# Kernel optimization log

Measured on AMD Instinct MI355X. Metric: run time of the kernel, lower is better.

The kernel has to match this reference:

```python
import jax, jax.numpy as jnp
import numpy as np

L, BS, D, NH = 1024, 4, 1024, 16
DH = D // NH
H = max(DH, L)  # big=True in DenseSynthesizer -> h = max(head_dim, n_tokens)


def setup_inputs() -> dict:
    key = jax.random.key(0)
    ks = jax.random.split(key, 10)
    s = 0.02
    x = jax.random.normal(ks[0], (L, BS, D), dtype=jnp.float32)
    # additive causal mask (n_tokens, n_tokens)
    causal = jnp.tril(jnp.ones((L, L), dtype=bool))
    attention_mask = jnp.where(causal, 0.0, -1e9).astype(jnp.float32)
    Wi = jax.random.normal(ks[1], (2 * D, D), dtype=jnp.float32) * s
    bi = jnp.zeros((2 * D,), dtype=jnp.float32)
    w1 = jax.random.normal(ks[2], (NH, DH, H), dtype=jnp.float32) * s
    b1 = jnp.zeros((NH, H), dtype=jnp.float32)
    w2 = jax.random.normal(ks[3], (NH, H, L), dtype=jnp.float32) * s
    b2 = jnp.zeros((NH, L), dtype=jnp.float32)
    Wo = jax.random.normal(ks[4], (D, D), dtype=jnp.float32) * s
    bo = jnp.zeros((D,), dtype=jnp.float32)
    return {"x": x, "attention_mask": attention_mask, "Wi": Wi, "bi": bi,
            "w1": w1, "b1": b1, "w2": w2, "b2": b2, "Wo": Wo, "bo": bo}


def reference(x, attention_mask, Wi, bi, w1, b1, w2, b2, Wo, bo):
    l, bs, d = x.shape
    nh, dh, h = w1.shape
    # input projection, chunk into synthesizer input q and values v
    proj = x @ Wi.T + bi                                    # (l, bs, 2d)
    q, v = jnp.split(proj, 2, axis=-1)
    q = q.reshape(l, bs, nh, dh).transpose(1, 0, 2, 3)      # (bs, l, nh, dh)
    v = v.reshape(l, bs * nh, dh).transpose(1, 0, 2)        # (bs*nh, l, dh), n = b*nh + k
    # DenseSynthesizer: per-head two-layer MLP producing attention logits
    hid = jax.nn.relu(jnp.einsum('blkd,kdh->blkh', q, w1) + b1)
    logits = jnp.einsum('blkh,khm->blkm', hid, w2) + b2     # (bs, l, nh, n_tokens)
    logits = logits[..., :l]
    # faithful to torch transpose(0,3).view(l,l,bs*nh).transpose(0,2):
    # flattened batch-head index is m = k*bs + b (head-major)
    logits = logits.transpose(2, 0, 1, 3).reshape(bs * nh, l, l)
    logits = logits + attention_mask[None, :, :]
    probs = jax.nn.softmax(logits, axis=-1)                 # dropout p=0 (eval)
    out = jnp.matmul(probs, v)                              # (bs*nh, l, dh)
    out = out.transpose(1, 0, 2).reshape(l, bs, d)
    return out @ Wo.T + bo
```

## Files before the change

### kernel.cpp

```cpp
#include <hip/hip_runtime.h>

typedef unsigned short u16;
typedef short bf16x8 __attribute__((ext_vector_type(8)));
typedef float f32x4 __attribute__((ext_vector_type(4)));

#define BSZ 4
#define DD 1024
#define LLL 1024

__device__ __forceinline__ float bf2f(u16 u) {
    union { unsigned int i; float f; } w;
    w.i = ((unsigned int)u) << 16;
    return w.f;
}
__device__ __forceinline__ u16 f2bf(float f) {
    union { float fl; unsigned int i; } w;
    w.fl = f;
    w.i += 0x7fffu + ((w.i >> 16) & 1u);
    return (u16)(w.i >> 16);
}

__device__ __forceinline__ void load_lds16(const u16* g, u16* l) {
    __builtin_amdgcn_global_load_lds(
        (const __attribute__((address_space(1))) unsigned int*)g,
        (__attribute__((address_space(3))) unsigned int*)l, 16, 0, 0);
}

__global__ void cvt_all(const float* __restrict__ x, const float* __restrict__ Wi,
                        const float* __restrict__ Wo, u16* __restrict__ xb,
                        u16* __restrict__ wib, u16* __restrict__ wob) {
    int b = blockIdx.x;
    const float* in; u16* out;
    if (b < 4096)      { in = x;  out = xb; }
    else if (b < 6144) { in = Wi; out = wib; b -= 4096; }
    else               { in = Wo; out = wob; b -= 6144; }
    const size_t i = ((size_t)b * 256 + threadIdx.x) * 4;
    const float4 v = *(const float4*)(in + i);
    ushort4 o;
    o.x = f2bf(v.x); o.y = f2bf(v.y); o.z = f2bf(v.z); o.w = f2bf(v.w);
    *(ushort4*)(out + i) = o;
}

__global__ void transpose_cvt(const float* __restrict__ in, u16* __restrict__ out,
                              int R, int C) {
    __shared__ float tile[32][33];
    const size_t base = (size_t)blockIdx.z * R * C;
    const int c0 = blockIdx.x << 5, r0 = blockIdx.y << 5;
    const int tx = threadIdx.x & 31, ty = threadIdx.x >> 5;
    #pragma unroll
    for (int i = 0; i < 32; i += 8)
        tile[ty + i][tx] = in[base + (size_t)(r0 + ty + i) * C + c0 + tx];
    __syncthreads();
    #pragma unroll
    for (int i = 0; i < 32; i += 8)
        out[base + (size_t)(c0 + ty + i) * R + r0 + tx] = f2bf(tile[tx][ty + i]);
}

__global__ void build_vt(const u16* __restrict__ proj, u16* __restrict__ vt) {
    __shared__ u16 tile[64][66];
    const int t = threadIdx.x;
    const int m0 = blockIdx.x << 6;
    const int jj = blockIdx.y;
    const int b = jj >> 4, k = jj & 15;
    const int tx = t & 63, ty = t >> 6;
    #pragma unroll
    for (int mi = ty; mi < 64; mi += 4)
        tile[mi][tx] = proj[(size_t)((m0 + mi) * BSZ + b) * 2048 + 1024 + k * 64 + tx];
    __syncthreads();
    #pragma unroll
    for (int di = ty; di < 64; di += 4)
        vt[((size_t)jj * 80 + di) * 1024 + m0 + tx] = tile[tx][di];
    #pragma unroll
    for (int di = 64 + ty; di < 80; di += 4)
        vt[((size_t)jj * 80 + di) * 1024 + m0 + tx] = (di == 64) ? 0x3F80 : 0;
}

template<int OUT_F32, int RELU>
__global__ __launch_bounds__(256, 2) void gemm_bf16_nt(
    const u16* __restrict__ A, int lda, long long sA,
    const u16* __restrict__ B, int ldb, long long sB,
    const float* __restrict__ bias, int sBias,
    void* __restrict__ C, int ldc, long long sC,
    int K)
{
    __shared__ u16 As[128 * 64];
    __shared__ u16 Bs[128 * 64];
    const int t = threadIdx.x;
    const int z = blockIdx.z;
    const u16* Ab = A + (size_t)z * sA + (size_t)blockIdx.x * 128 * lda;
    const u16* Bb = B + (size_t)z * sB + (size_t)blockIdx.y * 128 * ldb;
    const int wave = t >> 6, lane = t & 63;
    const int wrow = (wave >> 1) << 6;
    const int wcol = (wave & 1) << 6;
    const int lr = lane & 15, lq = lane >> 4;
    const int srow = t >> 3;
    const int gchunk = (t & 7) ^ (srow & 7);
    const u16* ApG = Ab + (size_t)srow * lda + gchunk * 8;
    const u16* BpG = Bb + (size_t)srow * ldb + gchunk * 8;
    u16* AsD = &As[t * 8];
    u16* BsD = &Bs[t * 8];
    const int o0 = ((lq    ) ^ (lr & 7)) * 8;
    const int o1 = ((lq + 4) ^ (lr & 7)) * 8;

    f32x4 acc[4][4];
    #pragma unroll
    for (int i = 0; i < 4; i++)
        #pragma unroll
        for (int j = 0; j < 4; j++)
            acc[i][j] = (f32x4){0.f, 0.f, 0.f, 0.f};

    for (int k0 = 0; k0 < K; k0 += 64) {
        __syncthreads();
        #pragma unroll
        for (int j = 0; j < 4; j++) {
            load_lds16(ApG + (size_t)j * 32 * lda + k0, AsD + j * 2048);
            load_lds16(BpG + (size_t)j * 32 * ldb + k0, BsD + j * 2048);
        }
        __syncthreads();
        #pragma unroll
        for (int s = 0; s < 2; s++) {
            const int oo = s ? o1 : o0;
            bf16x8 af[4], bfv[4];
            #pragma unroll
            for (int i = 0; i < 4; i++)
                af[i] = *(const bf16x8*)&As[(wrow + i * 16 + lr) * 64 + oo];
            #pragma unroll
            for (int j = 0; j < 4; j++)
                bfv[j] = *(const bf16x8*)&Bs[(wcol + j * 16 + lr) * 64 + oo];
            #pragma unroll
            for (int i = 0; i < 4; i++)
                #pragma unroll
                for (int j = 0; j < 4; j++)
                    acc[i][j] = __builtin_amdgcn_mfma_f32_16x16x32_bf16(
                        af[i], bfv[j], acc[i][j], 0, 0, 0);
        }
    }

    const float* biasb = bias + (size_t)z * sBias;
    const size_t row0 = (size_t)blockIdx.x * 128 + wrow + lq * 4;
    const int col0 = blockIdx.y * 128 + wcol + lr;
    #pragma unroll
    for (int j = 0; j < 4; j++) {
        const int col = col0 + j * 16;
        const float bb = biasb[col];
        #pragma unroll
        for (int i = 0; i < 4; i++) {
            #pragma unroll
            for (int r = 0; r < 4; r++) {
                const size_t row = row0 + i * 16 + r;
                float v = acc[i][j][r] + bb;
                if (RELU) v = fmaxf(v, 0.f);
                const size_t idx = row * (size_t)ldc + col;
                if (OUT_F32) ((float*)C)[(size_t)z * sC + idx] = v;
                else         ((u16*)C)[(size_t)z * sC + idx] = f2bf(v);
            }
        }
    }
}

__global__ __launch_bounds__(256, 2) void fused_attn(
    const u16* __restrict__ hid,
    const u16* __restrict__ w2t,
    const float* __restrict__ b2,
    const u16* __restrict__ vt,
    u16* __restrict__ attn)
{
    __shared__ u16 As[64 * 64];
    __shared__ u16 Bs[128 * 64];
    __shared__ u16 Ps[64 * 136];
    const int t = threadIdx.x;
    const int kq = blockIdx.x;
    const int pair = blockIdx.y;
    const int wave = t >> 6, lane = t & 63;
    const int lr = lane & 15, lq = lane >> 4;
    const int wi = wave >> 1, wj = wave & 1;
    const int srow = t >> 3;
    const int gch = (t & 7) ^ (srow & 7);
    const int o0 = ((lq    ) ^ (lr & 7)) * 8;
    const int o1 = ((lq + 4) ^ (lr & 7)) * 8;
    const int bv = kq >> 2;
    const int kvb = 4 * (kq & 3);
    const u16* hb = hid + (size_t)kq * 4194304;
    const u16* wb = w2t + (size_t)kq * 1048576 + (size_t)srow * 1024 + gch * 8;
    const float* b2b = b2 + kq * 1024;

    for (int part = 0; part < 2; part++) {
        const int s = part ? (63 - pair) : pair;
        const int l0 = s << 4;
        const int nt = (s >> 3) + 1;
        const u16* ApG0 = hb + (size_t)((l0 + (srow & 15)) * 4 + (srow >> 4)) * 1024 + gch * 8;
        const u16* ApG1 = ApG0 + (size_t)2 * 1024;
        f32x4 o[2][5];
        #pragma unroll
        for (int i = 0; i < 2; i++)
            #pragma unroll
            for (int j = 0; j < 5; j++)
                o[i][j] = (f32x4){0.f, 0.f, 0.f, 0.f};

        for (int mt = 0; mt < nt; mt++) {
            f32x4 acc[2][4];
            #pragma unroll
            for (int i = 0; i < 2; i++)
                #pragma unroll
                for (int j = 0; j < 4; j++)
                    acc[i][j] = (f32x4){0.f, 0.f, 0.f, 0.f};
            for (int k0 = 0; k0 < 1024; k0 += 64) {
                __syncthreads();
                load_lds16(ApG0 + k0, &As[t * 8]);
                load_lds16(ApG1 + k0, &As[t * 8 + 2048]);
                #pragma unroll
                for (int j2 = 0; j2 < 4; j2++)
                    load_lds16(wb + (size_t)(mt * 128 + j2 * 32) * 1024 + k0,
                               &Bs[j2 * 2048 + t * 8]);
                __syncthreads();
                #pragma unroll
                for (int s2 = 0; s2 < 2; s2++) {
                    const int oo = s2 ? o1 : o0;
                    bf16x8 af[2], bfv[4];
                    #pragma unroll
                    for (int i = 0; i < 2; i++)
                        af[i] = *(const bf16x8*)&As[(wi * 32 + i * 16 + lr) * 64 + oo];
                    #pragma unroll
                    for (int j = 0; j < 4; j++)
                        bfv[j] = *(const bf16x8*)&Bs[(wj * 64 + j * 16 + lr) * 64 + oo];
                    #pragma unroll
                    for (int i = 0; i < 2; i++)
                        #pragma unroll
                        for (int j = 0; j < 4; j++)
                            acc[i][j] = __builtin_amdgcn_mfma_f32_16x16x32_bf16(
                                af[i], bfv[j], acc[i][j], 0, 0, 0);
                }
            }
            __syncthreads();
            const int l = l0 + lq * 4;
            float b2v[4];
            #pragma unroll
            for (int j = 0; j < 4; j++)
                b2v[j] = b2b[mt * 128 + wj * 64 + j * 16 + lr];
            #pragma unroll
            for (int i = 0; i < 2; i++) {
                #pragma unroll
                for (int j = 0; j < 4; j++) {
                    const int cp = wj * 64 + j * 16 + lr;
                    const int m = mt * 128 + cp;
                    #pragma unroll
                    for (int rr = 0; rr < 4; rr++) {
                        const int rt = wi * 32 + i * 16 + lq * 4 + rr;
                        const float e = __expf(acc[i][j][rr] + b2v[j]);
                        Ps[rt * 136 + cp] = (m <= l + rr) ? f2bf(e) : (u16)0;
                    }
                }
            }
            __syncthreads();
            #pragma unroll
            for (int i = 0; i < 2; i++) {
                const int bq = 2 * wi + i;
                const u16* vbb = vt + (size_t)(kq * 4 + bq) * 80 * 1024
                               + (size_t)mt * 128 + lq * 8;
                #pragma unroll
                for (int kc = 0; kc < 4; kc++) {
                    const bf16x8 a = *(const bf16x8*)
                        &Ps[(wi * 32 + i * 16 + lr) * 136 + kc * 32 + lq * 8];
                    #pragma unroll
                    for (int j = 0; j < 5; j++) {
                        const bf16x8 b = *(const bf16x8*)
                            (vbb + (size_t)(j * 16 + lr) * 1024 + kc * 32);
                        o[i][j] = __builtin_amdgcn_mfma_f32_16x16x32_bf16(
                            a, b, o[i][j], 0, 0, 0);
                    }
                }
            }
        }
        #pragma unroll
        for (int i = 0; i < 2; i++) {
            const int bq = 2 * wi + i;
            float sden[4];
            #pragma unroll
            for (int rr = 0; rr < 4; rr++)
                sden[rr] = __shfl(o[i][4][rr], lq << 4);
            #pragma unroll
            for (int j = 0; j < 4; j++) {
                #pragma unroll
                for (int rr = 0; rr < 4; rr++) {
                    const int l = l0 + lq * 4 + rr;
                    attn[(size_t)(l * BSZ + bv) * 1024 + (kvb + bq) * 64 + j * 16 + lr]
                        = f2bf(o[i][j][rr] / sden[rr]);
                }
            }
        }
    }
}

extern "C" void kernel_launch(void* const* d_in, const int* in_sizes, int n_in,
                              void* d_out, int out_size, void* d_ws, size_t ws_size,
                              hipStream_t stream)
{
    (void)in_sizes; (void)n_in; (void)out_size; (void)ws_size;
    const float* x  = (const float*)d_in[0];
    const float* Wi = (const float*)d_in[2];
    const float* bi = (const float*)d_in[3];
    const float* w1 = (const float*)d_in[4];
    const float* b1 = (const float*)d_in[5];
    const float* w2 = (const float*)d_in[6];
    const float* b2 = (const float*)d_in[7];
    const float* Wo = (const float*)d_in[8];
    const float* bo = (const float*)d_in[9];

    u16* x_b    = (u16*)d_ws;
    u16* Wi_b   = x_b    + (size_t)4194304;
    u16* w1t    = Wi_b   + (size_t)2097152;
    u16* w2t    = w1t    + (size_t)1048576;
    u16* Wo_b   = w2t    + (size_t)16777216;
    u16* proj_b = Wo_b   + (size_t)1048576;
    u16* attn_b = proj_b + (size_t)8388608;
    u16* vt     = attn_b + (size_t)4194304;
    u16* hid_a  = vt     + (size_t)5242880;

    cvt_all<<<7168, 256, 0, stream>>>(x, Wi, Wo, x_b, Wi_b, Wo_b);
    transpose_cvt<<<dim3(32,  2, 16), 256, 0, stream>>>(w1, w1t, 64,   1024);
    transpose_cvt<<<dim3(32, 32, 16), 256, 0, stream>>>(w2, w2t, 1024, 1024);

    gemm_bf16_nt<0, 0><<<dim3(32, 16, 1), 256, 0, stream>>>(
        x_b, 1024, 0, Wi_b, 1024, 0, bi, 0, (void*)proj_b, 2048, 0, 1024);

    build_vt<<<dim3(16, 64), 256, 0, stream>>>(proj_b, vt);

    gemm_bf16_nt<0, 1><<<dim3(32, 8, 16), 256, 0, stream>>>(
        proj_b, 2048, 64,
        w1t, 64, 65536,
        b1, 1024,
        (void*)hid_a, 1024, 4194304, 64);

    fused_attn<<<dim3(16, 32), 256, 0, stream>>>(hid_a, w2t, b2, vt, attn_b);

    gemm_bf16_nt<1, 0><<<dim3(32, 8, 1), 256, 0, stream>>>(
        attn_b, 1024, 0, Wo_b, 1024, 0, bo, 0, d_out, 1024, 0, 1024);
}
```

Before: 439.5 us.

## Widen fused attention key tile to 256 and give each wave its own head

The fused synthesizer-attention kernel now processes 256 key columns per tile instead of 128. Each wave computes a 32x128 logit block per k-step, reusing each A fragment across twice as many MFMAs and halving the number of tile iterations and barriers. The PV stage is reorganised so each wave owns one 16-row head slice and accumulates a single output array. The cost is more causal-masked waste at tile granularity, larger LDS (Bs and Ps double, which may cut occupancy below 2 blocks per CU), and more accumulator registers.

After: 397.6 us. -9.5%, faster.

```diff
diff --git a/kernel.cpp b/kernel.cpp
--- a/kernel.cpp
+++ b/kernel.cpp
@@ -166,8 +166,8 @@
     u16* __restrict__ attn)
 {
     __shared__ u16 As[64 * 64];
-    __shared__ u16 Bs[128 * 64];
-    __shared__ u16 Ps[64 * 136];
+    __shared__ u16 Bs[256 * 64];
+    __shared__ u16 Ps[64 * 264];
     const int t = threadIdx.x;
     const int kq = blockIdx.x;
     const int pair = blockIdx.y;
@@ -187,104 +187,99 @@
     for (int part = 0; part < 2; part++) {
         const int s = part ? (63 - pair) : pair;
         const int l0 = s << 4;
-        const int nt = (s >> 3) + 1;
+        const int nt = (s >> 4) + 1;
         const u16* ApG0 = hb + (size_t)((l0 + (srow & 15)) * 4 + (srow >> 4)) * 1024 + gch * 8;
         const u16* ApG1 = ApG0 + (size_t)2 * 1024;
-        f32x4 o[2][5];
-        #pragma unroll
-        for (int i = 0; i < 2; i++)
-            #pragma unroll
-            for (int j = 0; j < 5; j++)
-                o[i][j] = (f32x4){0.f, 0.f, 0.f, 0.f};
+        f32x4 o[5];
+        #pragma unroll
+        for (int j = 0; j < 5; j++) o[j] = (f32x4){0.f, 0.f, 0.f, 0.f};
 
         for (int mt = 0; mt < nt; mt++) {
-            f32x4 acc[2][4];
+            f32x4 acc[2][8];
             #pragma unroll
             for (int i = 0; i < 2; i++)
                 #pragma unroll
-                for (int j = 0; j < 4; j++)
+                for (int j = 0; j < 8; j++)
                     acc[i][j] = (f32x4){0.f, 0.f, 0.f, 0.f};
             for (int k0 = 0; k0 < 1024; k0 += 64) {
                 __syncthreads();
                 load_lds16(ApG0 + k0, &As[t * 8]);
                 load_lds16(ApG1 + k0, &As[t * 8 + 2048]);
                 #pragma unroll
-                for (int j2 = 0; j2 < 4; j2++)
-                    load_lds16(wb + (size_t)(mt * 128 + j2 * 32) * 1024 + k0,
+                for (int j2 = 0; j2 < 8; j2++)
+                    load_lds16(wb + (size_t)(mt * 256 + j2 * 32) * 1024 + k0,
                                &Bs[j2 * 2048 + t * 8]);
                 __syncthreads();
                 #pragma unroll
                 for (int s2 = 0; s2 < 2; s2++) {
                     const int oo = s2 ? o1 : o0;
-                    bf16x8 af[2], bfv[4];
+                    bf16x8 af[2], bfv[8];
                     #pragma unroll
                     for (int i = 0; i < 2; i++)
                         af[i] = *(const bf16x8*)&As[(wi * 32 + i * 16 + lr) * 64 + oo];
                     #pragma unroll
-                    for (int j = 0; j < 4; j++)
-                        bfv[j] = *(const bf16x8*)&Bs[(wj * 64 + j * 16 + lr) * 64 + oo];
+                    for (int j = 0; j < 8; j++)
+                        bfv[j] = *(const bf16x8*)
+                            &Bs[(wj * 128 + j * 16 + lr) * 64 + oo];
                     #pragma unroll
                     for (int i = 0; i < 2; i++)
                         #pragma unroll
-                        for (int j = 0; j < 4; j++)
+                        for (int j = 0; j < 8; j++)
                             acc[i][j] = __builtin_amdgcn_mfma_f32_16x16x32_bf16(
                                 af[i], bfv[j], acc[i][j], 0, 0, 0);
                 }
             }
             __syncthreads();
-            const int l = l0 + lq * 4;
-            float b2v[4];
-            #pragma unroll
-            for (int j = 0; j < 4; j++)
-                b2v[j] = b2b[mt * 128 + wj * 64 + j * 16 + lr];
+            float b2v[8];
+            #pragma unroll
+            for (int j = 0; j < 8; j++)
+                b2v[j] = b2b[mt * 256 + wj * 128 + j * 16 + lr];
             #pragma unroll
             for (int i = 0; i < 2; i++) {
                 #pragma unroll
-                for (int j = 0; j < 4; j++) {
-                    const int cp = wj * 64 + j * 16 + lr;
-                    const int m = mt * 128 + cp;
+                for (int j = 0; j < 8; j++) {
+                    const int cp = wj * 128 + j * 16 + lr;
+                    const int m = mt * 256 + cp;
                     #pragma unroll
                     for (int rr = 0; rr < 4; rr++) {
                         const int rt = wi * 32 + i * 16 + lq * 4 + rr;
+                        const int l = l0 + lq * 4 + rr;
                         const float e = __expf(acc[i][j][rr] + b2v[j]);
-                        Ps[rt * 136 + cp] = (m <= l + rr) ? f2bf(e) : (u16)0;
+                        Ps[rt * 264 + cp] = (m <= l) ? f2bf(e) : (u16)0;
                     }
                 }
             }
             __syncthreads();
-            #pragma unroll
-            for (int i = 0; i < 2; i++) {
-                const int bq = 2 * wi + i;
-                const u16* vbb = vt + (size_t)(kq * 4 + bq) * 80 * 1024
-                               + (size_t)mt * 128 + lq * 8;
-                #pragma unroll
-                for (int kc = 0; kc < 4; kc++) {
+            {
+                const u16* vbb = vt + (size_t)(kq * 4 + wave) * 80 * 1024
+                               + (size_t)mt * 256 + lq * 8;
+                #pragma unroll
+                for (int kc = 0; kc < 8; kc++) {
                     const bf16x8 a = *(const bf16x8*)
-                        &Ps[(wi * 32 + i * 16 + lr) * 136 + kc * 32 + lq * 8];
+                        &Ps[(wave * 16 + lr) * 264 + kc * 32 + lq * 8];
                     #pragma unroll
                     for (int j = 0; j < 5; j++) {
                         const bf16x8 b = *(const bf16x8*)
                             (vbb + (size_t)(j * 16 + lr) * 1024 + kc * 32);
-                        o[i][j] = __builtin_amdgcn_mfma_f32_16x16x32_bf16(
-                            a, b, o[i][j], 0, 0, 0);
+                        o[j] = __builtin_amdgcn_mfma_f32_16x16x32_bf16(
+                            a, b, o[j], 0, 0, 0);
                     }
                 }
             }
         }
-        #pragma unroll
-        for (int i = 0; i < 2; i++) {
-            const int bq = 2 * wi + i;
+        {
+            const int bq = wave;
             float sden[4];
             #pragma unroll
             for (int rr = 0; rr < 4; rr++)
-                sden[rr] = __shfl(o[i][4][rr], lq << 4);
+                sden[rr] = __shfl(o[4][rr], lq << 4);
             #pragma unroll
             for (int j = 0; j < 4; j++) {
                 #pragma unroll
                 for (int rr = 0; rr < 4; rr++) {
                     const int l = l0 + lq * 4 + rr;
                     attn[(size_t)(l * BSZ + bv) * 1024 + (kvb + bq) * 64 + j * 16 + lr]
-                        = f2bf(o[i][j][rr] / sden[rr]);
+                        = f2bf(o[j][rr] / sden[rr]);
                 }
             }
         }
```
